# Performance work log

Hardware: AMD Instinct MI355X
Metric: run time of the kernel (lower is better)

## Reference

```python
import jax, jax.numpy as jnp
import numpy as np

D_MODEL = 1024
N_HEADS = 16
HEAD_DIM = D_MODEL // N_HEADS


def setup_inputs() -> dict:
    key = jax.random.key(0)
    ks = jax.random.split(key, 9)
    B, T = 2, 2048
    s = 1.0 / np.sqrt(D_MODEL)
    inp = {
        "x": jax.random.normal(ks[0], (B, T, D_MODEL), dtype=jnp.float32),
        "w_q": jax.random.normal(ks[1], (D_MODEL, D_MODEL), dtype=jnp.float32) * s,
        "b_q": jnp.zeros((D_MODEL,), dtype=jnp.float32),
        "w_k": jax.random.normal(ks[2], (D_MODEL, D_MODEL), dtype=jnp.float32) * s,
        "b_k": jnp.zeros((D_MODEL,), dtype=jnp.float32),
        "w_v": jax.random.normal(ks[3], (D_MODEL, D_MODEL), dtype=jnp.float32) * s,
        "b_v": jnp.zeros((D_MODEL,), dtype=jnp.float32),
        "w_o": jax.random.normal(ks[4], (D_MODEL, D_MODEL), dtype=jnp.float32) * s,
        "b_o": jnp.zeros((D_MODEL,), dtype=jnp.float32),
    }
    return inp


def reference(x, w_q, b_q, w_k, b_k, w_v, b_v, w_o, b_o):
    B, T, C = x.shape
    H, Dh = N_HEADS, HEAD_DIM
    # projections (weights stored as [out,in] like torch Linear -> x @ W.T + b)
    q = (x @ w_q.T + b_q).reshape(B, T, H, Dh).transpose(0, 2, 1, 3)  # [B,H,T,Dh]
    k = (x @ w_k.T + b_k).reshape(B, T, H, Dh).transpose(0, 2, 1, 3)
    v = (x @ w_v.T + b_v).reshape(B, T, H, Dh).transpose(0, 2, 1, 3)
    scale = 1.0 / jnp.sqrt(jnp.asarray(Dh, dtype=x.dtype))
    scores = jnp.einsum("bhqd,bhkd->bhqk", q, k) * scale  # [B,H,T,T]
    causal = jnp.tril(jnp.ones((T, T), dtype=bool))
    scores = jnp.where(causal[None, None], scores, jnp.asarray(-jnp.inf, dtype=scores.dtype))
    attn = jax.nn.softmax(scores, axis=-1)
    out = jnp.einsum("bhqk,bhkd->bhqd", attn, v)  # [B,H,T,Dh]
    out = out.transpose(0, 2, 1, 3).reshape(B, T, C)
    return out @ w_o.T + b_o
```

## Files before the change

kernel.cpp:

```cpp
#include <hip/hip_runtime.h>
#include <hip/hip_bf16.h>
#include <math.h>

#define BATCH 2
#define SEQ   2048
#define DMODEL 1024
#define NHEADS 16
#define HDIM  64
#define MROWS (BATCH*SEQ)
#define QSCALE 0.1803368801111204f

typedef __attribute__((ext_vector_type(8))) short bfr8;
typedef __attribute__((ext_vector_type(4))) float f32x4;

__device__ inline unsigned short f2bf(float f) {
    union { float f; unsigned u; } v; v.f = f;
    unsigned r = v.u + 0x7FFFu + ((v.u >> 16) & 1u);
    return (unsigned short)(r >> 16);
}

__device__ inline unsigned pack2bf(float a, float b) {
    union { __hip_bfloat162 h; unsigned u; } cv;
    cv.h = __float22bfloat162_rn(float2{a, b});
    return cv.u;
}

__device__ inline void gload16(const unsigned short* g, unsigned short* l) {
    __builtin_amdgcn_global_load_lds((const __attribute__((address_space(1))) void*)g,
        (__attribute__((address_space(3))) void*)l, 16, 0, 0);
}

__global__ __launch_bounds__(256) void cast_bf16(const float* __restrict__ in,
                                                 unsigned short* __restrict__ out, int n) {
    int i = (blockIdx.x * 256 + threadIdx.x) * 4;
    const int stride = gridDim.x * 256 * 4;
    for (; i < n; i += stride) {
        float4 v = *(const float4*)(in + i);
        ushort4 o;
        o.x = f2bf(v.x); o.y = f2bf(v.y); o.z = f2bf(v.z); o.w = f2bf(v.w);
        *(ushort4*)(out + i) = o;
    }
}

__global__ __launch_bounds__(256) void cast4_bf16(
    const float* __restrict__ a, const float* __restrict__ b,
    const float* __restrict__ c, const float* __restrict__ d,
    unsigned short* __restrict__ out) {
    const int NW = 1 << 20;
    int i = (blockIdx.x * 256 + threadIdx.x) * 4;
    const int stride = gridDim.x * 256 * 4;
    for (; i < 4 * NW; i += stride) {
        const int seg = i >> 20;
        const float* src = seg == 0 ? a : seg == 1 ? b : seg == 2 ? c : d;
        float4 v = *(const float4*)(src + (i & (NW - 1)));
        ushort4 o;
        o.x = f2bf(v.x); o.y = f2bf(v.y); o.z = f2bf(v.z); o.w = f2bf(v.w);
        *(ushort4*)(out + i) = o;
    }
}

template<int BM, int MODE>
__global__ __launch_bounds__(256) void gemm_bf16(
    const unsigned short* __restrict__ A, const unsigned short* __restrict__ W,
    const float* __restrict__ b0, const float* __restrict__ b1,
    const float* __restrict__ b2, void* __restrict__ Y)
{
    __shared__ __align__(16) unsigned short As[2][4][BM][8];
    __shared__ __align__(16) unsigned short Bs[2][4][128][8];

    const int tid = threadIdx.x;
    const int l = tid & 63, w = tid >> 6;
    const int wr = w >> 1, wc = w & 1;
    const int m0 = blockIdx.y * BM, n0 = blockIdx.x * 128;
    const int r15 = l & 15, g = l >> 4;
    constexpr int MR = BM / 32;

    f32x4 acc[MR][4] = {};

    auto stage = [&](int buf, int k0) {
        #pragma unroll
        for (int s = 0; s < BM / 64; ++s) {
            int idx = s * 256 + tid;
            int row = idx % BM, kg = idx / BM;
            gload16(A + (size_t)(m0 + row) * 1024 + k0 + kg * 8, &As[buf][kg][row][0]);
        }
        #pragma unroll
        for (int s = 0; s < 2; ++s) {
            int idx = s * 256 + tid;
            int row = idx & 127, kg = idx >> 7;
            gload16(W + (size_t)(n0 + row) * 1024 + k0 + kg * 8, &Bs[buf][kg][row][0]);
        }
    };

    stage(0, 0);
    __syncthreads();

    for (int t = 0; t < 32; ++t) {
        const int buf = t & 1;
        if (t + 1 < 32) stage(buf ^ 1, (t + 1) * 32);
        bfr8 a[MR], b[4];
        #pragma unroll
        for (int m = 0; m < MR; ++m)
            a[m] = *(const bfr8*)&As[buf][g][wr * (BM / 2) + m * 16 + r15][0];
        #pragma unroll
        for (int n = 0; n < 4; ++n)
            b[n] = *(const bfr8*)&Bs[buf][g][wc * 64 + n * 16 + r15][0];
        #pragma unroll
        for (int m = 0; m < MR; ++m)
            #pragma unroll
            for (int n = 0; n < 4; ++n)
                acc[m][n] = __builtin_amdgcn_mfma_f32_16x16x32_bf16(a[m], b[n], acc[m][n], 0, 0, 0);
        __syncthreads();
    }

    const size_t NX = (size_t)MROWS * DMODEL;
    #pragma unroll
    for (int m = 0; m < MR; ++m) {
        const int rowb = m0 + wr * (BM / 2) + m * 16 + g * 4;
        #pragma unroll
        for (int n = 0; n < 4; ++n) {
            const int col = n0 + wc * 64 + n * 16 + r15;
            const int proj = col >> 10, within = col & 1023;
            const float bc = (MODE == 2) ? b0[col]
                           : (proj == 0 ? b0[within] : proj == 1 ? b1[within] : b2[within]);
            #pragma unroll
            for (int i = 0; i < 4; ++i) {
                float v = acc[m][n][i] + bc;
                const int rr = rowb + i;
                if (MODE == 2) {
                    ((float*)Y)[(size_t)rr * 1024 + col] = v;
                } else {
                    if (proj == 0) v *= QSCALE;
                    const int bb = rr >> 11, tt = rr & 2047;
                    const int hh = within >> 6, dd = within & 63;
                    unsigned short* dst = (unsigned short*)Y + (size_t)proj * NX;
                    size_t idx;
                    if (proj < 2)
                        idx = (((size_t)bb * NHEADS + hh) * SEQ + tt) * HDIM + dd;
                    else
                        idx = (((size_t)bb * NHEADS + hh) * HDIM + dd) * SEQ + tt;
                    dst[idx] = f2bf(v);
                }
            }
        }
    }
}

__global__ __launch_bounds__(256, 2) void attn_mfma(
    const unsigned short* __restrict__ Q, const unsigned short* __restrict__ K,
    const unsigned short* __restrict__ VT, unsigned short* __restrict__ O)
{
    __shared__ __align__(16) unsigned short Ks[2][64][64];
    __shared__ __align__(16) unsigned short Vs[2][64][64];
    __shared__ __align__(16) unsigned short Ps[4][2][16][8][8];

    const int tid = threadIdx.x;
    const int l = tid & 63, w = tid >> 6;
    const int r15 = l & 15, g2 = (l >> 4) & 3;
    const int q0 = SEQ - 128 - blockIdx.x * 128;
    const int qw = q0 + w * 32;
    const int bh = blockIdx.y;

    const unsigned short* Qb = Q + (size_t)bh * SEQ * HDIM;
    const unsigned short* Kb = K + (size_t)bh * SEQ * HDIM;
    const unsigned short* Vb = VT + (size_t)bh * HDIM * SEQ;

    bfr8 qf[2][2];
    #pragma unroll
    for (int rf = 0; rf < 2; ++rf)
        #pragma unroll
        for (int ks = 0; ks < 2; ++ks)
            qf[rf][ks] = *(const bfr8*)(Qb + (size_t)(qw + rf * 16 + r15) * HDIM + ks * 32 + g2 * 8);

    auto stage = [&](int buf, int kv0) {
        #pragma unroll
        for (int s = 0; s < 2; ++s) {
            int idx = s * 256 + tid;
            int row = idx >> 3, gs = idx & 7;
            gload16(Kb + (size_t)(kv0 + row) * HDIM + ((gs ^ (row & 7)) * 8), &Ks[buf][row][gs * 8]);
            gload16(Vb + (size_t)row * SEQ + kv0 + ((gs ^ (row & 7)) * 8), &Vs[buf][row][gs * 8]);
        }
    };

    f32x4 o[4][2] = {};
    float mrow[2] = {-INFINITY, -INFINITY}, lrow[2] = {0.f, 0.f};

    const int ntiles = q0 / 64 + 2;
    stage(0, 0);
    __syncthreads();

    for (int kt = 0; kt < ntiles; ++kt) {
        const int kv0 = kt * 64, buf = kt & 1;
        if (kt + 1 < ntiles) stage(buf ^ 1, kv0 + 64);

        f32x4 s[4][2];
        #pragma unroll
        for (int c = 0; c < 4; ++c) {
            const int rk = c * 16 + r15;
            const bfr8 kf0 = *(const bfr8*)&Ks[buf][rk][(g2 ^ (r15 & 7)) * 8];
            const bfr8 kf1 = *(const bfr8*)&Ks[buf][rk][((4 + g2) ^ (r15 & 7)) * 8];
            #pragma unroll
            for (int rf = 0; rf < 2; ++rf) {
                f32x4 z = {0.f, 0.f, 0.f, 0.f};
                z = __builtin_amdgcn_mfma_f32_16x16x32_bf16(kf0, qf[rf][0], z, 0, 0, 0);
                s[c][rf] = __builtin_amdgcn_mfma_f32_16x16x32_bf16(kf1, qf[rf][1], z, 0, 0, 0);
            }
        }

        if (kt >= ntiles - 2) {
            #pragma unroll
            for (int c = 0; c < 4; ++c)
                #pragma unroll
                for (int rf = 0; rf < 2; ++rf) {
                    const int q = qw + rf * 16 + r15;
                    #pragma unroll
                    for (int i = 0; i < 4; ++i)
                        if (kv0 + c * 16 + g2 * 4 + i > q) s[c][rf][i] = -INFINITY;
                }
        }

        float scl[2];
        #pragma unroll
        for (int rf = 0; rf < 2; ++rf) {
            float tm = s[0][rf][0];
            #pragma unroll
            for (int c = 0; c < 4; ++c)
                #pragma unroll
                for (int i = 0; i < 4; ++i) tm = fmaxf(tm, s[c][rf][i]);
            tm = fmaxf(tm, __shfl_xor(tm, 16));
            tm = fmaxf(tm, __shfl_xor(tm, 32));
            const float mn = fmaxf(mrow[rf], tm);
            scl[rf] = exp2f(mrow[rf] - mn);
            mrow[rf] = mn;
            float ls = 0.f;
            #pragma unroll
            for (int c = 0; c < 4; ++c)
                #pragma unroll
                for (int i = 0; i < 4; ++i) {
                    const float p = exp2f(s[c][rf][i] - mn);
                    s[c][rf][i] = p;
                    ls += p;
                }
            ls += __shfl_xor(ls, 16);
            ls += __shfl_xor(ls, 32);
            lrow[rf] = lrow[rf] * scl[rf] + ls;
            #pragma unroll
            for (int c = 0; c < 4; ++c) {
                const int kgw = (c * 2 + (g2 >> 1)) ^ (r15 & 7);
                #pragma unroll
                for (int p = 0; p < 2; ++p) {
                    unsigned pk = pack2bf(s[c][rf][2 * p], s[c][rf][2 * p + 1]);
                    *(unsigned*)&Ps[w][rf][r15][kgw][(g2 & 1) * 4 + 2 * p] = pk;
                }
            }
        }

        #pragma unroll
        for (int rf = 0; rf < 2; ++rf) {
            float sb[4];
            #pragma unroll
            for (int i = 0; i < 4; ++i) sb[i] = __shfl(scl[rf], g2 * 4 + i, 16);
            #pragma unroll
            for (int ch = 0; ch < 4; ++ch)
                #pragma unroll
                for (int i = 0; i < 4; ++i) o[ch][rf][i] *= sb[i];
        }
        bfr8 pf[2][2];
        #pragma unroll
        for (int rf = 0; rf < 2; ++rf)
            #pragma unroll
            for (int ks = 0; ks < 2; ++ks)
                pf[rf][ks] = *(const bfr8*)&Ps[w][rf][r15][(ks * 4 + g2) ^ (r15 & 7)][0];
        #pragma unroll
        for (int ch = 0; ch < 4; ++ch) {
            const int d = ch * 16 + r15;
            const bfr8 vf0 = *(const bfr8*)&Vs[buf][d][(g2 ^ (r15 & 7)) * 8];
            const bfr8 vf1 = *(const bfr8*)&Vs[buf][d][((4 + g2) ^ (r15 & 7)) * 8];
            #pragma unroll
            for (int rf = 0; rf < 2; ++rf) {
                o[ch][rf] = __builtin_amdgcn_mfma_f32_16x16x32_bf16(pf[rf][0], vf0, o[ch][rf], 0, 0, 0);
                o[ch][rf] = __builtin_amdgcn_mfma_f32_16x16x32_bf16(pf[rf][1], vf1, o[ch][rf], 0, 0, 0);
            }
        }
        __syncthreads();
    }

    const int b = bh >> 4, h = bh & 15;
    #pragma unroll
    for (int rf = 0; rf < 2; ++rf) {
        const float inv = 1.f / lrow[rf];
        float ib[4];
        #pragma unroll
        for (int i = 0; i < 4; ++i) ib[i] = __shfl(inv, g2 * 4 + i, 16);
        #pragma unroll
        for (int i = 0; i < 4; ++i) {
            const int row = qw + rf * 16 + g2 * 4 + i;
            #pragma unroll
            for (int ch = 0; ch < 4; ++ch) {
                const int col = h * HDIM + ch * 16 + r15;
                O[((size_t)b * SEQ + row) * DMODEL + col] = f2bf(o[ch][rf][i] * ib[i]);
            }
        }
    }
}

extern "C" void kernel_launch(void* const* d_in, const int* in_sizes, int n_in,
                              void* d_out, int out_size, void* d_ws, size_t ws_size,
                              hipStream_t stream) {
    const float* x   = (const float*)d_in[0];
    const float* w_q = (const float*)d_in[1];
    const float* b_q = (const float*)d_in[2];
    const float* w_k = (const float*)d_in[3];
    const float* b_k = (const float*)d_in[4];
    const float* w_v = (const float*)d_in[5];
    const float* b_v = (const float*)d_in[6];
    const float* w_o = (const float*)d_in[7];
    const float* b_o = (const float*)d_in[8];
    float* out = (float*)d_out;

    const size_t NX = (size_t)MROWS * DMODEL;
    const size_t NW = (size_t)DMODEL * DMODEL;
    unsigned short* xb    = (unsigned short*)d_ws;
    unsigned short* wcomb = xb + NX;
    unsigned short* wob   = wcomb + 3 * NW;
    unsigned short* Qw    = wob + NW;
    unsigned short* Kw    = Qw + NX;
    unsigned short* VTw   = Kw + NX;
    unsigned short* Ow    = VTw + NX;

    cast_bf16<<<1024, 256, 0, stream>>>(x, xb, (int)NX);
    cast4_bf16<<<2048, 256, 0, stream>>>(w_q, w_k, w_v, w_o, wcomb);

    gemm_bf16<128, 0><<<dim3(24, 32), 256, 0, stream>>>(xb, wcomb, b_q, b_k, b_v, Qw);

    attn_mfma<<<dim3(16, 32), 256, 0, stream>>>(Qw, Kw, VTw, Ow);

    gemm_bf16<64, 2><<<dim3(8, 64), 256, 0, stream>>>(Ow, wob, b_o, nullptr, nullptr, out);
}
```

Measured before the change: 190.9 us.

## Triple-buffer GEMM, swizzle blocks across XCDs, and drop LDS staging in attention

The GEMM moves to a three-stage LDS ring with explicit vmcnt waits and one barrier per k-step, and for the QKV projection it remaps block indices so neighbouring tiles land on the same XCD. The attention kernel stops staging K/V through shared memory and reads fragments directly from global/L2. It trims causal tiles per wave, skips the online-softmax rescale unless the max grows by more than a threshold, transposes the PV MFMA operands so the output is written as packed vectors, and rotates q-block order per head for load balance. Costs: direct global loads in attention rely on cache hits and the lazy rescale slightly changes numerics, while the occupancy hint of 2 on attention was removed.

```diff
diff --git a/kernel.cpp b/kernel.cpp
--- a/kernel.cpp
+++ b/kernel.cpp
@@ -65,19 +65,33 @@
     const float* __restrict__ b0, const float* __restrict__ b1,
     const float* __restrict__ b2, void* __restrict__ Y)
 {
-    __shared__ __align__(16) unsigned short As[2][4][BM][8];
-    __shared__ __align__(16) unsigned short Bs[2][4][128][8];
+    __shared__ __align__(16) unsigned short As[3][4][BM][8];
+    __shared__ __align__(16) unsigned short Bs[3][4][128][8];
+
+    constexpr int NT  = 32;
+    constexpr int NLD = BM / 64 + 2;
 
     const int tid = threadIdx.x;
     const int l = tid & 63, w = tid >> 6;
     const int wr = w >> 1, wc = w & 1;
-    const int m0 = blockIdx.y * BM, n0 = blockIdx.x * 128;
     const int r15 = l & 15, g = l >> 4;
     constexpr int MR = BM / 32;
 
+    int bx, by;
+    if (MODE == 0) {
+        const int flat = blockIdx.x + blockIdx.y * 24;
+        const int xcd = flat & 7, s = flat >> 3;
+        bx = (xcd & 1) * 12 + s % 12;
+        by = (xcd >> 1) * 8 + s / 12;
+    } else {
+        bx = blockIdx.x; by = blockIdx.y;
+    }
+    const int m0 = by * BM, n0 = bx * 128;
+
     f32x4 acc[MR][4] = {};
 
-    auto stage = [&](int buf, int k0) {
+    auto stage = [&](int buf, int t) {
+        const int k0 = t * 32;
         #pragma unroll
         for (int s = 0; s < BM / 64; ++s) {
             int idx = s * 256 + tid;
@@ -93,11 +107,16 @@
     };
 
     stage(0, 0);
-    __syncthreads();
-
-    for (int t = 0; t < 32; ++t) {
-        const int buf = t & 1;
-        if (t + 1 < 32) stage(buf ^ 1, (t + 1) * 32);
+    stage(1, 1);
+
+    for (int t = 0; t < NT; ++t) {
+        if (t < NT - 1)
+            asm volatile("s_waitcnt vmcnt(%0)\ns_barrier" :: "n"(NLD) : "memory");
+        else
+            asm volatile("s_waitcnt vmcnt(0)\ns_barrier" ::: "memory");
+        if (t + 2 < NT) stage((t + 2) % 3, t + 2);
+
+        const int buf = t % 3;
         bfr8 a[MR], b[4];
         #pragma unroll
         for (int m = 0; m < MR; ++m)
@@ -110,7 +129,6 @@
             #pragma unroll
             for (int n = 0; n < 4; ++n)
                 acc[m][n] = __builtin_amdgcn_mfma_f32_16x16x32_bf16(a[m], b[n], acc[m][n], 0, 0, 0);
-        __syncthreads();
     }
 
     const size_t NX = (size_t)MROWS * DMODEL;
@@ -146,20 +164,19 @@
     }
 }
 
-__global__ __launch_bounds__(256, 2) void attn_mfma(
+__global__ __launch_bounds__(256) void attn_mfma(
     const unsigned short* __restrict__ Q, const unsigned short* __restrict__ K,
     const unsigned short* __restrict__ VT, unsigned short* __restrict__ O)
 {
-    __shared__ __align__(16) unsigned short Ks[2][64][64];
-    __shared__ __align__(16) unsigned short Vs[2][64][64];
-    __shared__ __align__(16) unsigned short Ps[4][2][16][8][8];
+    __shared__ __align__(16) unsigned short Ps[4][2][8][16][8];
 
     const int tid = threadIdx.x;
     const int l = tid & 63, w = tid >> 6;
-    const int r15 = l & 15, g2 = (l >> 4) & 3;
-    const int q0 = SEQ - 128 - blockIdx.x * 128;
-    const int qw = q0 + w * 32;
+    const int r15 = l & 15, g2 = l >> 4;
     const int bh = blockIdx.y;
+    const int qi = (blockIdx.x + bh) & 15;
+    const int qbase = SEQ - 128 - qi * 128;
+    const int qw = qbase + w * 32;
 
     const unsigned short* Qb = Q + (size_t)bh * SEQ * HDIM;
     const unsigned short* Kb = K + (size_t)bh * SEQ * HDIM;
@@ -172,33 +189,19 @@
         for (int ks = 0; ks < 2; ++ks)
             qf[rf][ks] = *(const bfr8*)(Qb + (size_t)(qw + rf * 16 + r15) * HDIM + ks * 32 + g2 * 8);
 
-    auto stage = [&](int buf, int kv0) {
-        #pragma unroll
-        for (int s = 0; s < 2; ++s) {
-            int idx = s * 256 + tid;
-            int row = idx >> 3, gs = idx & 7;
-            gload16(Kb + (size_t)(kv0 + row) * HDIM + ((gs ^ (row & 7)) * 8), &Ks[buf][row][gs * 8]);
-            gload16(Vb + (size_t)row * SEQ + kv0 + ((gs ^ (row & 7)) * 8), &Vs[buf][row][gs * 8]);
-        }
-    };
-
     f32x4 o[4][2] = {};
-    float mrow[2] = {-INFINITY, -INFINITY}, lrow[2] = {0.f, 0.f};
-
-    const int ntiles = q0 / 64 + 2;
-    stage(0, 0);
-    __syncthreads();
-
+    float m[2] = {-INFINITY, -INFINITY}, rden[2] = {0.f, 0.f};
+
+    const int ntiles = qw / 64 + 1;
     for (int kt = 0; kt < ntiles; ++kt) {
-        const int kv0 = kt * 64, buf = kt & 1;
-        if (kt + 1 < ntiles) stage(buf ^ 1, kv0 + 64);
+        const int kv0 = kt * 64;
 
         f32x4 s[4][2];
         #pragma unroll
         for (int c = 0; c < 4; ++c) {
-            const int rk = c * 16 + r15;
-            const bfr8 kf0 = *(const bfr8*)&Ks[buf][rk][(g2 ^ (r15 & 7)) * 8];
-            const bfr8 kf1 = *(const bfr8*)&Ks[buf][rk][((4 + g2) ^ (r15 & 7)) * 8];
+            const unsigned short* kr = Kb + (size_t)(kv0 + c * 16 + r15) * HDIM;
+            const bfr8 kf0 = *(const bfr8*)(kr + g2 * 8);
+            const bfr8 kf1 = *(const bfr8*)(kr + 32 + g2 * 8);
             #pragma unroll
             for (int rf = 0; rf < 2; ++rf) {
                 f32x4 z = {0.f, 0.f, 0.f, 0.f};
@@ -207,7 +210,7 @@
             }
         }
 
-        if (kt >= ntiles - 2) {
+        if (kt == ntiles - 1) {
             #pragma unroll
             for (int c = 0; c < 4; ++c)
                 #pragma unroll
@@ -219,87 +222,85 @@
                 }
         }
 
-        float scl[2];
+        float tm[2];
         #pragma unroll
         for (int rf = 0; rf < 2; ++rf) {
-            float tm = s[0][rf][0];
-            #pragma unroll
-            for (int c = 0; c < 4; ++c)
+            float t0 = fmaxf(fmaxf(s[0][rf][0], s[0][rf][1]), fmaxf(s[0][rf][2], s[0][rf][3]));
+            #pragma unroll
+            for (int c = 1; c < 4; ++c)
                 #pragma unroll
-                for (int i = 0; i < 4; ++i) tm = fmaxf(tm, s[c][rf][i]);
-            tm = fmaxf(tm, __shfl_xor(tm, 16));
-            tm = fmaxf(tm, __shfl_xor(tm, 32));
-            const float mn = fmaxf(mrow[rf], tm);
-            scl[rf] = exp2f(mrow[rf] - mn);
-            mrow[rf] = mn;
+                for (int i = 0; i < 4; ++i) t0 = fmaxf(t0, s[c][rf][i]);
+            t0 = fmaxf(t0, __shfl_xor(t0, 16));
+            t0 = fmaxf(t0, __shfl_xor(t0, 32));
+            tm[rf] = t0;
+        }
+        if (__any(fmaxf(tm[0] - m[0], tm[1] - m[1]) > 8.f)) {
+            #pragma unroll
+            for (int rf = 0; rf < 2; ++rf) {
+                const float mn = fmaxf(m[rf], tm[rf]);
+                const float scl = exp2f(m[rf] - mn);
+                m[rf] = mn;
+                rden[rf] *= scl;
+                #pragma unroll
+                for (int ch = 0; ch < 4; ++ch)
+                    #pragma unroll
+                    for (int i = 0; i < 4; ++i) o[ch][rf][i] *= scl;
+            }
+        }
+        #pragma unroll
+        for (int rf = 0; rf < 2; ++rf) {
             float ls = 0.f;
             #pragma unroll
             for (int c = 0; c < 4; ++c)
                 #pragma unroll
                 for (int i = 0; i < 4; ++i) {
-                    const float p = exp2f(s[c][rf][i] - mn);
+                    const float p = exp2f(s[c][rf][i] - m[rf]);
                     s[c][rf][i] = p;
                     ls += p;
                 }
             ls += __shfl_xor(ls, 16);
             ls += __shfl_xor(ls, 32);
-            lrow[rf] = lrow[rf] * scl[rf] + ls;
+            rden[rf] += ls;
+            const int eb = (g2 & 1) * 4;
             #pragma unroll
             for (int c = 0; c < 4; ++c) {
-                const int kgw = (c * 2 + (g2 >> 1)) ^ (r15 & 7);
-                #pragma unroll
-                for (int p = 0; p < 2; ++p) {
-                    unsigned pk = pack2bf(s[c][rf][2 * p], s[c][rf][2 * p + 1]);
-                    *(unsigned*)&Ps[w][rf][r15][kgw][(g2 & 1) * 4 + 2 * p] = pk;
-                }
-            }
-        }
-
-        #pragma unroll
-        for (int rf = 0; rf < 2; ++rf) {
-            float sb[4];
-            #pragma unroll
-            for (int i = 0; i < 4; ++i) sb[i] = __shfl(scl[rf], g2 * 4 + i, 16);
-            #pragma unroll
-            for (int ch = 0; ch < 4; ++ch)
-                #pragma unroll
-                for (int i = 0; i < 4; ++i) o[ch][rf][i] *= sb[i];
+                const int kg = c * 2 + (g2 >> 1);
+                *(unsigned*)&Ps[w][rf][kg][r15][eb]     = pack2bf(s[c][rf][0], s[c][rf][1]);
+                *(unsigned*)&Ps[w][rf][kg][r15][eb + 2] = pack2bf(s[c][rf][2], s[c][rf][3]);
+            }
         }
         bfr8 pf[2][2];
         #pragma unroll
         for (int rf = 0; rf < 2; ++rf)
             #pragma unroll
             for (int ks = 0; ks < 2; ++ks)
-                pf[rf][ks] = *(const bfr8*)&Ps[w][rf][r15][(ks * 4 + g2) ^ (r15 & 7)][0];
+                pf[rf][ks] = *(const bfr8*)&Ps[w][rf][ks * 4 + g2][r15][0];
+
         #pragma unroll
         for (int ch = 0; ch < 4; ++ch) {
-            const int d = ch * 16 + r15;
-            const bfr8 vf0 = *(const bfr8*)&Vs[buf][d][(g2 ^ (r15 & 7)) * 8];
-            const bfr8 vf1 = *(const bfr8*)&Vs[buf][d][((4 + g2) ^ (r15 & 7)) * 8];
+            const unsigned short* vr = Vb + (size_t)(ch * 16 + r15) * SEQ + kv0;
+            const bfr8 vf0 = *(const bfr8*)(vr + g2 * 8);
+            const bfr8 vf1 = *(const bfr8*)(vr + 32 + g2 * 8);
             #pragma unroll
             for (int rf = 0; rf < 2; ++rf) {
-                o[ch][rf] = __builtin_amdgcn_mfma_f32_16x16x32_bf16(pf[rf][0], vf0, o[ch][rf], 0, 0, 0);
-                o[ch][rf] = __builtin_amdgcn_mfma_f32_16x16x32_bf16(pf[rf][1], vf1, o[ch][rf], 0, 0, 0);
-            }
-        }
-        __syncthreads();
+                o[ch][rf] = __builtin_amdgcn_mfma_f32_16x16x32_bf16(vf0, pf[rf][0], o[ch][rf], 0, 0, 0);
+                o[ch][rf] = __builtin_amdgcn_mfma_f32_16x16x32_bf16(vf1, pf[rf][1], o[ch][rf], 0, 0, 0);
+            }
+        }
     }
 
     const int b = bh >> 4, h = bh & 15;
     #pragma unroll
     for (int rf = 0; rf < 2; ++rf) {
-        const float inv = 1.f / lrow[rf];
-        float ib[4];
-        #pragma unroll
-        for (int i = 0; i < 4; ++i) ib[i] = __shfl(inv, g2 * 4 + i, 16);
-        #pragma unroll
-        for (int i = 0; i < 4; ++i) {
-            const int row = qw + rf * 16 + g2 * 4 + i;
-            #pragma unroll
-            for (int ch = 0; ch < 4; ++ch) {
-                const int col = h * HDIM + ch * 16 + r15;
-                O[((size_t)b * SEQ + row) * DMODEL + col] = f2bf(o[ch][rf][i] * ib[i]);
-            }
+        const float inv = 1.f / rden[rf];
+        const int q = qw + rf * 16 + r15;
+        unsigned short* Ob = O + ((size_t)b * SEQ + q) * DMODEL + h * HDIM + g2 * 4;
+        #pragma unroll
+        for (int ch = 0; ch < 4; ++ch) {
+            uint2 pk;
+            pk.x = pack2bf(o[ch][rf][0] * inv, o[ch][rf][1] * inv);
+            pk.y = pack2bf(o[ch][rf][2] * inv, o[ch][rf][3] * inv);
+            *(uint2*)(Ob + ch * 16) = pk;
         }
     }
 }
```

Result: slower. 226.9 us (+18.9%).
